# Kernel tuning notes

Hardware: AMD Instinct MI355X
Metric: run time of the kernel (lower is better)

The kernel has to match this reference:

```python
import jax, jax.numpy as jnp
import numpy as np

N_Q = 4
DEPTH = 6
DIM = 16  # 2**N_Q

# ---- fixed `design` dict (forward arg in the torch module; fixed here so the
# gate sequence is static, exercising every gate branch) ----
_K1 = ['x', 'y', 'z']
_K2 = ['H', 'Px', 'Py', 'Pz', 'CNot', 'CZ', 'Tof', 'CSwap']
DESIGN = {}
for _l in range(DEPTH):
    for _n in range(N_Q):
        DESIGN[str(_l) + str(_n) + '0'] = ((_l + _n) % 2 == 0)
        DESIGN[str(_l) + str(_n) + '1'] = _K1[(_l + _n) % 3]
        DESIGN[str(_l) + str(_n) + '2'] = _K2[(_l * N_Q + _n) % 8]

# ---- elementary gate matrices (numpy, build-time) ----
_H = np.array([[1, 1], [1, -1]], np.complex64) / np.sqrt(2.0)
_X = np.array([[0, 1], [1, 0]], np.complex64)
_Y = np.array([[0, -1j], [1j, 0]], np.complex64)
_Z = np.array([[1, 0], [0, -1]], np.complex64)
_CNOT = np.eye(4, dtype=np.complex64)[[0, 1, 3, 2]]
_CZ = np.diag(np.array([1, 1, 1, -1], np.complex64))
_TOF = np.eye(8, dtype=np.complex64)[[0, 1, 2, 3, 4, 5, 7, 6]]
_CSWAP = np.eye(8, dtype=np.complex64)[[0, 1, 2, 3, 4, 6, 5, 7]]


def _embed(gate, wires):
    # Embed a 2^k x 2^k gate acting on `wires` (wire 0 = most-significant bit,
    # PennyLane convention) into a full 16x16 unitary.
    k = len(wires)
    U = np.zeros((DIM, DIM), np.complex64)
    for i in range(DIM):
        bits = [(i >> (N_Q - 1 - q)) & 1 for q in range(N_Q)]
        sub_in = 0
        for w in wires:
            sub_in = (sub_in << 1) | bits[w]
        for sub_out in range(2 ** k):
            amp = gate[sub_out, sub_in]
            if amp != 0:
                ob = list(bits)
                for j, w in enumerate(wires):
                    ob[w] = (sub_out >> (k - 1 - j)) & 1
                o = 0
                for q in range(N_Q):
                    o = (o << 1) | ob[q]
                U[o, i] += amp
    return jnp.asarray(U)


# ---- static op list: ('fix', U16) | ('rot', kind, wire, angle_source) ----
_G1 = {'H': _H, 'Px': _X, 'Py': _Y, 'Pz': _Z}
OPS = [('fix', _embed(_H, [q])) for q in range(N_Q)]  # initial Hadamards
for _l in range(DEPTH):
    for _n in range(N_Q):
        if DESIGN[str(_l) + str(_n) + '0']:
            OPS.append(('rot', 'y', _n, ('x', _n)))  # RY(input feature)
        OPS.append(('rot', DESIGN[str(_l) + str(_n) + '1'], _n, ('w', _l, _n)))
        g = DESIGN[str(_l) + str(_n) + '2']
        if g in _G1:
            OPS.append(('fix', _embed(_G1[g], [_n])))
        elif g == 'CNot':
            OPS.append(('fix', _embed(_CNOT, [_n, (_n + 1) % N_Q])))
        elif g == 'CZ':
            OPS.append(('fix', _embed(_CZ, [_n, (_n + 1) % N_Q])))
        elif g == 'Tof':
            OPS.append(('fix', _embed(_TOF, [_n, (_n + 1) % N_Q, (_n + 2) % N_Q])))
        elif g == 'CSwap':
            OPS.append(('fix', _embed(_CSWAP, [_n, (_n + 1) % N_Q, (_n + 2) % N_Q])))


def _rot_mat(kind, th):
    # th: (B,) real angles -> (B,2,2) complex64 rotation matrices
    half = 0.5 * th
    c = jnp.cos(half).astype(jnp.complex64)
    s = jnp.sin(half).astype(jnp.complex64)
    if kind == 'x':
        m = [[c, (-1j) * s], [(-1j) * s, c]]
    elif kind == 'y':
        m = [[c, -s], [s, c]]
    else:  # 'z'
        e = jnp.exp((-1j) * half.astype(jnp.complex64))
        z = jnp.zeros_like(e)
        m = [[e, z], [z, jnp.conj(e)]]
    return jnp.stack([jnp.stack(m[0], -1), jnp.stack(m[1], -1)], -2)


def _apply_1q(state, M, q):
    # state: (B,16) complex, M: (B,2,2) complex, single-qubit gate on wire q
    B = state.shape[0]
    s = state.reshape(B, 2 ** q, 2, 2 ** (N_Q - 1 - q))
    s = jnp.einsum('bij,bajc->baic', M, s)
    return s.reshape(B, DIM)


def _run(state, x, w, adjoint):
    # adjoint: reversed gate order, negated rotation angles; all fixed gates
    # here (H, Paulis, CNOT, CZ, Toffoli, CSWAP) are Hermitian => self-adjoint.
    sign = -1.0 if adjoint else 1.0
    B = state.shape[0]
    for op in (reversed(OPS) if adjoint else OPS):
        if op[0] == 'fix':
            state = jnp.einsum('ij,bj->bi', op[1], state)
        else:
            _, kind, wire, src = op
            th = x[:, src[1]] if src[0] == 'x' else jnp.broadcast_to(w[src[1], src[2]], (B,))
            state = _apply_1q(state, _rot_mat(kind, sign * th), wire)
    return state


def _forward(x1, x2, q_params):
    w = q_params.reshape(DEPTH, N_Q)
    B = x1.shape[0]
    state = jnp.zeros((B, DIM), jnp.complex64).at[:, 0].set(1.0)
    state = _run(state, x1, w, False)   # quantum_net(x1, w)
    state = _run(state, x2, w, True)    # adjoint(quantum_net)(x2, w)
    a = state[:, 0]                     # probs[0] = |<0...0|psi>|^2
    return a.real ** 2 + a.imag ** 2


def setup_inputs():
    key = jax.random.key(0)
    k1, k2, k3 = jax.random.split(key, 3)
    B = 262144
    return {
        'x1': jax.random.normal(k1, (B, N_Q), jnp.float32),
        'x2': jax.random.normal(k2, (B, N_Q), jnp.float32),
        'q_params': jax.random.normal(k3, (DEPTH * N_Q,), jnp.float32),
    }


def reference(x1, x2, q_params):
    return _forward(x1, x2, q_params)
```

## Files before the change

### kernel.cpp

```cpp
#include <hip/hip_runtime.h>
#include <math.h>


#define DEVI static __device__ __forceinline__

typedef float f2 __attribute__((ext_vector_type(2)));

DEVI f2 nI(f2 a) { f2 r; r.x = a.y; r.y = -a.x; return r; }
DEVI f2 pI(f2 a) { f2 r; r.x = -a.y; r.y = a.x; return r; }


template<int Q> DEVI void gH(f2* v) {
  constexpr int m = 1 << (3 - Q);
  const float K = 0.70710678118654752440f;
#pragma unroll
  for (int i = 0; i < 16; ++i) if (!(i & m)) {
    const int j = i | m;
    f2 a = v[i], b = v[j];
    v[i] = (a + b) * K;
    v[j] = (a - b) * K;
  }
}

template<int Q> DEVI void gX(f2* v) {
  constexpr int m = 1 << (3 - Q);
#pragma unroll
  for (int i = 0; i < 16; ++i) if (!(i & m)) {
    const int j = i | m;
    f2 t = v[i]; v[i] = v[j]; v[j] = t;
  }
}

template<int Q> DEVI void gY(f2* v) {
  constexpr int m = 1 << (3 - Q);
#pragma unroll
  for (int i = 0; i < 16; ++i) if (!(i & m)) {
    const int j = i | m;
    f2 a = v[i], b = v[j];
    v[i] = nI(b);
    v[j] = pI(a);
  }
}

template<int Q> DEVI void gZ(f2* v) {
  constexpr int m = 1 << (3 - Q);
#pragma unroll
  for (int i = 0; i < 16; ++i) if (i & m) v[i] = -v[i];
}

template<int Q> DEVI void gRY(f2* v, float c, float s) {
  constexpr int m = 1 << (3 - Q);
#pragma unroll
  for (int i = 0; i < 16; ++i) if (!(i & m)) {
    const int j = i | m;
    f2 a = v[i], b = v[j];
    v[i] = a * c - b * s;
    v[j] = a * s + b * c;
  }
}

template<int Q> DEVI void gRX(f2* v, float c, float s) {
  constexpr int m = 1 << (3 - Q);
#pragma unroll
  for (int i = 0; i < 16; ++i) if (!(i & m)) {
    const int j = i | m;
    f2 a = v[i], b = v[j];
    v[i] = a * c + nI(b) * s;
    v[j] = b * c + nI(a) * s;
  }
}

template<int Q> DEVI void gRZ(f2* v, float c, float s) {
  constexpr int m = 1 << (3 - Q);
#pragma unroll
  for (int i = 0; i < 16; ++i) {
    f2 a = v[i];
    if (i & m) v[i] = a * c - nI(a) * s;
    else       v[i] = a * c + nI(a) * s;
  }
}

template<int C, int T> DEVI void gCNOT(f2* v) {
  constexpr int mc = 1 << (3 - C), mt = 1 << (3 - T);
#pragma unroll
  for (int i = 0; i < 16; ++i) if ((i & mc) && !(i & mt)) {
    const int j = i | mt;
    f2 t = v[i]; v[i] = v[j]; v[j] = t;
  }
}

template<int A, int B2> DEVI void gCZ(f2* v) {
  constexpr int ma = 1 << (3 - A), mb = 1 << (3 - B2);
#pragma unroll
  for (int i = 0; i < 16; ++i) if ((i & ma) && (i & mb)) v[i] = -v[i];
}

template<int C1, int C2, int T> DEVI void gTOF(f2* v) {
  constexpr int m1 = 1 << (3 - C1), m2 = 1 << (3 - C2), mt = 1 << (3 - T);
#pragma unroll
  for (int i = 0; i < 16; ++i) if ((i & m1) && (i & m2) && !(i & mt)) {
    const int j = i | mt;
    f2 t = v[i]; v[i] = v[j]; v[j] = t;
  }
}

template<int C, int A, int B2> DEVI void gCSWAP(f2* v) {
  constexpr int mc = 1 << (3 - C), ma = 1 << (3 - A), mb = 1 << (3 - B2);
#pragma unroll
  for (int i = 0; i < 16; ++i) if ((i & mc) && (i & ma) && !(i & mb)) {
    const int j = (i ^ ma) | mb;
    f2 t = v[i]; v[i] = v[j]; v[j] = t;
  }
}

DEVI float rlane(float v, int l) {
  return __int_as_float(__builtin_amdgcn_readlane(__float_as_int(v), l));
}

__global__ __launch_bounds__(256)
void qsim(const float* __restrict__ x1, const float* __restrict__ x2,
          const float* __restrict__ q, float* __restrict__ out, int B)
{
  const int b = blockIdx.x * blockDim.x + threadIdx.x;
  if (b >= B) return;

  const int lane = threadIdx.x & 63;
  float qv = 0.f;
  if (lane < 24) qv = q[lane];
  float mys, myc;
  sincosf(0.5f * qv, &mys, &myc);
  float cw[24], sw[24];
#pragma unroll
  for (int k = 0; k < 24; ++k) { cw[k] = rlane(myc, k); sw[k] = rlane(mys, k); }

  const float4 xa = reinterpret_cast<const float4*>(x1)[b];
  const float4 xb = reinterpret_cast<const float4*>(x2)[b];
  float ca[4], sa[4], cb[4], sb[4];
  __sincosf(0.5f * xa.x, &sa[0], &ca[0]);
  __sincosf(0.5f * xa.y, &sa[1], &ca[1]);
  __sincosf(0.5f * xa.z, &sa[2], &ca[2]);
  __sincosf(0.5f * xa.w, &sa[3], &ca[3]);
  __sincosf(0.5f * xb.x, &sb[0], &cb[0]);
  __sincosf(0.5f * xb.y, &sb[1], &cb[1]);
  __sincosf(0.5f * xb.z, &sb[2], &cb[2]);
  __sincosf(0.5f * xb.w, &sb[3], &cb[3]);

  f2 v[16];
#pragma unroll
  for (int i = 0; i < 16; ++i) { v[i].x = 0.f; v[i].y = 0.f; }
  v[0].x = 1.f;

  gH<0>(v); gH<1>(v); gH<2>(v); gH<3>(v);
  gRY<0>(v, ca[0], sa[0]); gRX<0>(v, cw[0],  sw[0]);  gH<0>(v);
  gRY<1>(v, cw[1], sw[1]); gX<1>(v);
  gRY<2>(v, ca[2], sa[2]); gRZ<2>(v, cw[2],  sw[2]);  gY<2>(v);
  gRX<3>(v, cw[3], sw[3]); gZ<3>(v);
  gRY<0>(v, cw[4], sw[4]); gCNOT<0,1>(v);
  gRY<1>(v, ca[1], sa[1]); gRZ<1>(v, cw[5],  sw[5]);  gCZ<1,2>(v);
  gRX<2>(v, cw[6], sw[6]); gTOF<2,3,0>(v);
  gRY<3>(v, ca[3], sa[3]); gRY<3>(v, cw[7],  sw[7]);  gCSWAP<3,0,1>(v);
  gRY<0>(v, ca[0], sa[0]); gRZ<0>(v, cw[8],  sw[8]);  gH<0>(v);
  gRX<1>(v, cw[9], sw[9]); gX<1>(v);
  gRY<2>(v, ca[2], sa[2]); gRY<2>(v, cw[10], sw[10]); gY<2>(v);
  gRZ<3>(v, cw[11], sw[11]); gZ<3>(v);
  gRX<0>(v, cw[12], sw[12]); gCNOT<0,1>(v);
  gRY<1>(v, ca[1], sa[1]); gRY<1>(v, cw[13], sw[13]); gCZ<1,2>(v);
  gRZ<2>(v, cw[14], sw[14]); gTOF<2,3,0>(v);
  gRY<3>(v, ca[3], sa[3]); gRX<3>(v, cw[15], sw[15]); gCSWAP<3,0,1>(v);
  gRY<0>(v, ca[0], sa[0]); gRY<0>(v, cw[16], sw[16]); gH<0>(v);
  gRZ<1>(v, cw[17], sw[17]); gX<1>(v);
  gRY<2>(v, ca[2], sa[2]); gRX<2>(v, cw[18], sw[18]); gY<2>(v);
  gRY<3>(v, cw[19], sw[19]); gZ<3>(v);
  gRZ<0>(v, cw[20], sw[20]); gCNOT<0,1>(v);
  gRY<1>(v, ca[1], sa[1]); gRX<1>(v, cw[21], sw[21]); gCZ<1,2>(v);
  gRY<2>(v, cw[22], sw[22]); gTOF<2,3,0>(v);
  gRY<3>(v, ca[3], sa[3]); gRZ<3>(v, cw[23], sw[23]); gCSWAP<3,0,1>(v);

  gCSWAP<3,0,1>(v); gRZ<3>(v, cw[23], -sw[23]); gRY<3>(v, cb[3], -sb[3]);
  gTOF<2,3,0>(v);   gRY<2>(v, cw[22], -sw[22]);
  gCZ<1,2>(v);      gRX<1>(v, cw[21], -sw[21]); gRY<1>(v, cb[1], -sb[1]);
  gCNOT<0,1>(v);    gRZ<0>(v, cw[20], -sw[20]);
  gZ<3>(v); gRY<3>(v, cw[19], -sw[19]);
  gY<2>(v); gRX<2>(v, cw[18], -sw[18]); gRY<2>(v, cb[2], -sb[2]);
  gX<1>(v); gRZ<1>(v, cw[17], -sw[17]);
  gH<0>(v); gRY<0>(v, cw[16], -sw[16]); gRY<0>(v, cb[0], -sb[0]);
  gCSWAP<3,0,1>(v); gRX<3>(v, cw[15], -sw[15]); gRY<3>(v, cb[3], -sb[3]);
  gTOF<2,3,0>(v);   gRZ<2>(v, cw[14], -sw[14]);
  gCZ<1,2>(v);      gRY<1>(v, cw[13], -sw[13]); gRY<1>(v, cb[1], -sb[1]);
  gCNOT<0,1>(v);    gRX<0>(v, cw[12], -sw[12]);
  gZ<3>(v); gRZ<3>(v, cw[11], -sw[11]);
  gY<2>(v); gRY<2>(v, cw[10], -sw[10]); gRY<2>(v, cb[2], -sb[2]);
  gX<1>(v); gRX<1>(v, cw[9],  -sw[9]);
  gH<0>(v); gRZ<0>(v, cw[8],  -sw[8]);  gRY<0>(v, cb[0], -sb[0]);
  gCSWAP<3,0,1>(v); gRY<3>(v, cw[7], -sw[7]); gRY<3>(v, cb[3], -sb[3]);
  gTOF<2,3,0>(v);   gRX<2>(v, cw[6], -sw[6]);
  gCZ<1,2>(v);      gRZ<1>(v, cw[5], -sw[5]); gRY<1>(v, cb[1], -sb[1]);
  gCNOT<0,1>(v);    gRY<0>(v, cw[4], -sw[4]);
  gZ<3>(v); gRX<3>(v, cw[3], -sw[3]);
  gY<2>(v); gRZ<2>(v, cw[2], -sw[2]); gRY<2>(v, cb[2], -sb[2]);
  gX<1>(v); gRY<1>(v, cw[1], -sw[1]);
  gH<0>(v); gRX<0>(v, cw[0], -sw[0]); gRY<0>(v, cb[0], -sb[0]);
  gH<3>(v); gH<2>(v); gH<1>(v); gH<0>(v);

  f2 a0 = v[0];
  out[b] = a0.x * a0.x + a0.y * a0.y;
}

extern "C" void kernel_launch(void* const* d_in, const int* in_sizes, int n_in,
                              void* d_out, int out_size, void* d_ws, size_t ws_size,
                              hipStream_t stream) {
  const float* x1 = (const float*)d_in[0];
  const float* x2 = (const float*)d_in[1];
  const float* q  = (const float*)d_in[2];
  float* out = (float*)d_out;
  const int B = in_sizes[0] / 4;
  const int block = 256;
  const int grid = (B + block - 1) / block;
  qsim<<<grid, block, 0, stream>>>(x1, x2, q, out, B);
}
```

Before: 85.15 us.

## Compute overlap as inner product of two forward states with fused gates

Instead of applying the forward circuit and then its adjoint, the kernel runs the forward circuit on both inputs and takes the inner product <U(x2)|U(x1)>. The initial Hadamards are folded into a uniform starting state, and adjacent gate pairs are fused into single kernels (H·RX, Y·RZ, Z·RX and others), including merged consecutive RY angles. Parameter sincos now uses the fast intrinsic, and launch bounds request higher occupancy. In exchange, two 16-amplitude states are live at once, which raises register pressure, and accuracy may shift slightly.

```diff
diff --git a/kernel.cpp b/kernel.cpp
--- a/kernel.cpp
+++ b/kernel.cpp
@@ -6,8 +6,9 @@
 
 typedef float f2 __attribute__((ext_vector_type(2)));
 
-DEVI f2 nI(f2 a) { f2 r; r.x = a.y; r.y = -a.x; return r; }
-DEVI f2 pI(f2 a) { f2 r; r.x = -a.y; r.y = a.x; return r; }
+DEVI f2 nI(f2 a) { f2 r; r.x = a.y;  r.y = -a.x; return r; }
+DEVI f2 pI(f2 a) { f2 r; r.x = -a.y; r.y = a.x;  return r; }
+DEVI f2 cmul(f2 a, f2 g) { return a * g.x + pI(a) * g.y; }
 
 
 template<int Q> DEVI void gH(f2* v) {
@@ -42,12 +43,6 @@
   }
 }
 
-template<int Q> DEVI void gZ(f2* v) {
-  constexpr int m = 1 << (3 - Q);
-#pragma unroll
-  for (int i = 0; i < 16; ++i) if (i & m) v[i] = -v[i];
-}
-
 template<int Q> DEVI void gRY(f2* v, float c, float s) {
   constexpr int m = 1 << (3 - Q);
 #pragma unroll
@@ -75,9 +70,107 @@
 #pragma unroll
   for (int i = 0; i < 16; ++i) {
     f2 a = v[i];
-    if (i & m) v[i] = a * c - nI(a) * s;
-    else       v[i] = a * c + nI(a) * s;
-  }
+    if (i & m) v[i] = a * c + pI(a) * s;
+    else       v[i] = a * c - pI(a) * s;
+  }
+}
+
+
+template<int Q> DEVI void gHRY(f2* v, float c, float s) {
+  constexpr int m = 1 << (3 - Q);
+  const float K = 0.70710678118654752440f;
+  const float al = K * (c + s), be = K * (c - s);
+#pragma unroll
+  for (int i = 0; i < 16; ++i) if (!(i & m)) {
+    const int j = i | m;
+    f2 a = v[i], b = v[j];
+    v[i] = a * al + b * be;
+    v[j] = a * be - b * al;
+  }
+}
+
+template<int Q> DEVI void gHRX(f2* v, f2 Em, f2 Ep) {
+  constexpr int m = 1 << (3 - Q);
+#pragma unroll
+  for (int i = 0; i < 16; ++i) if (!(i & m)) {
+    const int j = i | m;
+    f2 a = v[i], b = v[j];
+    f2 t = a + b, u = a - b;
+    v[i] = cmul(t, Em);
+    v[j] = cmul(u, Ep);
+  }
+}
+
+template<int Q> DEVI void gHRZ(f2* v, f2 Em, f2 Ep) {
+  constexpr int m = 1 << (3 - Q);
+#pragma unroll
+  for (int i = 0; i < 16; ++i) if (!(i & m)) {
+    const int j = i | m;
+    f2 a = v[i], b = v[j];
+    f2 p = cmul(a, Em), q = cmul(b, Ep);
+    v[i] = p + q;
+    v[j] = p - q;
+  }
+}
+
+template<int Q> DEVI void gYRZ(f2* v, f2 G1, f2 G2) {
+  constexpr int m = 1 << (3 - Q);
+#pragma unroll
+  for (int i = 0; i < 16; ++i) if (!(i & m)) {
+    const int j = i | m;
+    f2 a = v[i], b = v[j];
+    v[i] = cmul(b, G1);
+    v[j] = cmul(a, G2);
+  }
+}
+
+template<int Q> DEVI void gYRX(f2* v, float c, float s) {
+  constexpr int m = 1 << (3 - Q);
+#pragma unroll
+  for (int i = 0; i < 16; ++i) if (!(i & m)) {
+    const int j = i | m;
+    f2 a = v[i], b = v[j];
+    v[i] = nI(b) * c - a * s;
+    v[j] = pI(a) * c + b * s;
+  }
+}
+
+template<int Q> DEVI void gZRX(f2* v, float c, float s) {
+  constexpr int m = 1 << (3 - Q);
+#pragma unroll
+  for (int i = 0; i < 16; ++i) if (!(i & m)) {
+    const int j = i | m;
+    f2 a = v[i], b = v[j];
+    v[i] = a * c + nI(b) * s;
+    v[j] = pI(a) * s - b * c;
+  }
+}
+
+template<int Q> DEVI void gZRZ(f2* v, float c, float s) {
+  constexpr int m = 1 << (3 - Q);
+#pragma unroll
+  for (int i = 0; i < 16; ++i) {
+    f2 a = v[i];
+    if (i & m) v[i] = pI(a) * (-s) - a * c;
+    else       v[i] = a * c - pI(a) * s;
+  }
+}
+
+template<int Q> DEVI void gZRY(f2* v, float c, float s) {
+  constexpr int m = 1 << (3 - Q);
+#pragma unroll
+  for (int i = 0; i < 16; ++i) if (!(i & m)) {
+    const int j = i | m;
+    f2 a = v[i], b = v[j];
+    v[i] = a * c - b * s;
+    v[j] = a * (-s) - b * c;
+  }
+}
+
+template<int A, int B2> DEVI void gCZ(f2* v) {
+  constexpr int ma = 1 << (3 - A), mb = 1 << (3 - B2);
+#pragma unroll
+  for (int i = 0; i < 16; ++i) if ((i & ma) && (i & mb)) v[i] = -v[i];
 }
 
 template<int C, int T> DEVI void gCNOT(f2* v) {
@@ -89,12 +182,6 @@
   }
 }
 
-template<int A, int B2> DEVI void gCZ(f2* v) {
-  constexpr int ma = 1 << (3 - A), mb = 1 << (3 - B2);
-#pragma unroll
-  for (int i = 0; i < 16; ++i) if ((i & ma) && (i & mb)) v[i] = -v[i];
-}
-
 template<int C1, int C2, int T> DEVI void gTOF(f2* v) {
   constexpr int m1 = 1 << (3 - C1), m2 = 1 << (3 - C2), mt = 1 << (3 - T);
 #pragma unroll
@@ -113,11 +200,51 @@
   }
 }
 
+struct Uni {
+  float cw[24], sw[24];
+  f2 Em0, Ep0;
+  f2 G1_2, G2_2;
+  f2 Em8, Ep8;
+};
+
+DEVI void fwd(f2* v, const float* cx, const float* sx, const Uni& U) {
+  const float* cw = U.cw; const float* sw = U.sw;
+  const float c73  = cx[3]*cw[7]  - sx[3]*sw[7],  s73  = sx[3]*cw[7]  + cx[3]*sw[7];
+  const float c102 = cx[2]*cw[10] - sx[2]*sw[10], s102 = sx[2]*cw[10] + cx[2]*sw[10];
+  const float c131 = cx[1]*cw[13] - sx[1]*sw[13], s131 = sx[1]*cw[13] + cx[1]*sw[13];
+  const float c160 = cx[0]*cw[16] - sx[0]*sw[16], s160 = sx[0]*cw[16] + cx[0]*sw[16];
+
+  gRY<0>(v, cx[0], sx[0]); gHRX<0>(v, U.Em0, U.Ep0);
+  gRY<1>(v, cw[1], sw[1]); gX<1>(v);
+  gRY<2>(v, cx[2], sx[2]); gYRZ<2>(v, U.G1_2, U.G2_2);
+  gZRX<3>(v, cw[3], sw[3]);
+  gRY<0>(v, cw[4], sw[4]); gCNOT<0,1>(v);
+  gRY<1>(v, cx[1], sx[1]); gRZ<1>(v, cw[5], sw[5]); gCZ<1,2>(v);
+  gRX<2>(v, cw[6], sw[6]); gTOF<2,3,0>(v);
+  gRY<3>(v, c73, s73);     gCSWAP<3,0,1>(v);
+  gRY<0>(v, cx[0], sx[0]); gHRZ<0>(v, U.Em8, U.Ep8);
+  gRX<1>(v, cw[9], sw[9]); gX<1>(v);
+  gRY<2>(v, c102, s102);   gY<2>(v);
+  gZRZ<3>(v, cw[11], sw[11]);
+  gRX<0>(v, cw[12], sw[12]); gCNOT<0,1>(v);
+  gRY<1>(v, c131, s131);     gCZ<1,2>(v);
+  gRZ<2>(v, cw[14], sw[14]); gTOF<2,3,0>(v);
+  gRY<3>(v, cx[3], sx[3]); gRX<3>(v, cw[15], sw[15]); gCSWAP<3,0,1>(v);
+  gHRY<0>(v, c160, s160);
+  gRZ<1>(v, cw[17], sw[17]); gX<1>(v);
+  gRY<2>(v, cx[2], sx[2]); gYRX<2>(v, cw[18], sw[18]);
+  gZRY<3>(v, cw[19], sw[19]);
+  gRZ<0>(v, cw[20], sw[20]); gCNOT<0,1>(v);
+  gRY<1>(v, cx[1], sx[1]); gRX<1>(v, cw[21], sw[21]); gCZ<1,2>(v);
+  gRY<2>(v, cw[22], sw[22]); gTOF<2,3,0>(v);
+  gRY<3>(v, cx[3], sx[3]); gRZ<3>(v, cw[23], sw[23]); gCSWAP<3,0,1>(v);
+}
+
 DEVI float rlane(float v, int l) {
   return __int_as_float(__builtin_amdgcn_readlane(__float_as_int(v), l));
 }
 
-__global__ __launch_bounds__(256)
+__global__ __launch_bounds__(256, 4)
 void qsim(const float* __restrict__ x1, const float* __restrict__ x2,
           const float* __restrict__ q, float* __restrict__ out, int B)
 {
@@ -128,10 +255,18 @@
   float qv = 0.f;
   if (lane < 24) qv = q[lane];
   float mys, myc;
-  sincosf(0.5f * qv, &mys, &myc);
-  float cw[24], sw[24];
-#pragma unroll
-  for (int k = 0; k < 24; ++k) { cw[k] = rlane(myc, k); sw[k] = rlane(mys, k); }
+  __sincosf(0.5f * qv, &mys, &myc);
+
+  Uni U;
+#pragma unroll
+  for (int k = 0; k < 24; ++k) { U.cw[k] = rlane(myc, k); U.sw[k] = rlane(mys, k); }
+  const float K = 0.70710678118654752440f;
+  U.Em0.x  = K * U.cw[0]; U.Em0.y  = -K * U.sw[0];
+  U.Ep0.x  = K * U.cw[0]; U.Ep0.y  =  K * U.sw[0];
+  U.G1_2.x = U.sw[2];     U.G1_2.y = -U.cw[2];
+  U.G2_2.x = U.sw[2];     U.G2_2.y =  U.cw[2];
+  U.Em8.x  = K * U.cw[8]; U.Em8.y  = -K * U.sw[8];
+  U.Ep8.x  = K * U.cw[8]; U.Ep8.y  =  K * U.sw[8];
 
   const float4 xa = reinterpret_cast<const float4*>(x1)[b];
   const float4 xb = reinterpret_cast<const float4*>(x2)[b];
@@ -145,65 +280,20 @@
   __sincosf(0.5f * xb.z, &sb[2], &cb[2]);
   __sincosf(0.5f * xb.w, &sb[3], &cb[3]);
 
-  f2 v[16];
-#pragma unroll
-  for (int i = 0; i < 16; ++i) { v[i].x = 0.f; v[i].y = 0.f; }
-  v[0].x = 1.f;
-
-  gH<0>(v); gH<1>(v); gH<2>(v); gH<3>(v);
-  gRY<0>(v, ca[0], sa[0]); gRX<0>(v, cw[0],  sw[0]);  gH<0>(v);
-  gRY<1>(v, cw[1], sw[1]); gX<1>(v);
-  gRY<2>(v, ca[2], sa[2]); gRZ<2>(v, cw[2],  sw[2]);  gY<2>(v);
-  gRX<3>(v, cw[3], sw[3]); gZ<3>(v);
-  gRY<0>(v, cw[4], sw[4]); gCNOT<0,1>(v);
-  gRY<1>(v, ca[1], sa[1]); gRZ<1>(v, cw[5],  sw[5]);  gCZ<1,2>(v);
-  gRX<2>(v, cw[6], sw[6]); gTOF<2,3,0>(v);
-  gRY<3>(v, ca[3], sa[3]); gRY<3>(v, cw[7],  sw[7]);  gCSWAP<3,0,1>(v);
-  gRY<0>(v, ca[0], sa[0]); gRZ<0>(v, cw[8],  sw[8]);  gH<0>(v);
-  gRX<1>(v, cw[9], sw[9]); gX<1>(v);
-  gRY<2>(v, ca[2], sa[2]); gRY<2>(v, cw[10], sw[10]); gY<2>(v);
-  gRZ<3>(v, cw[11], sw[11]); gZ<3>(v);
-  gRX<0>(v, cw[12], sw[12]); gCNOT<0,1>(v);
-  gRY<1>(v, ca[1], sa[1]); gRY<1>(v, cw[13], sw[13]); gCZ<1,2>(v);
-  gRZ<2>(v, cw[14], sw[14]); gTOF<2,3,0>(v);
-  gRY<3>(v, ca[3], sa[3]); gRX<3>(v, cw[15], sw[15]); gCSWAP<3,0,1>(v);
-  gRY<0>(v, ca[0], sa[0]); gRY<0>(v, cw[16], sw[16]); gH<0>(v);
-  gRZ<1>(v, cw[17], sw[17]); gX<1>(v);
-  gRY<2>(v, ca[2], sa[2]); gRX<2>(v, cw[18], sw[18]); gY<2>(v);
-  gRY<3>(v, cw[19], sw[19]); gZ<3>(v);
-  gRZ<0>(v, cw[20], sw[20]); gCNOT<0,1>(v);
-  gRY<1>(v, ca[1], sa[1]); gRX<1>(v, cw[21], sw[21]); gCZ<1,2>(v);
-  gRY<2>(v, cw[22], sw[22]); gTOF<2,3,0>(v);
-  gRY<3>(v, ca[3], sa[3]); gRZ<3>(v, cw[23], sw[23]); gCSWAP<3,0,1>(v);
-
-  gCSWAP<3,0,1>(v); gRZ<3>(v, cw[23], -sw[23]); gRY<3>(v, cb[3], -sb[3]);
-  gTOF<2,3,0>(v);   gRY<2>(v, cw[22], -sw[22]);
-  gCZ<1,2>(v);      gRX<1>(v, cw[21], -sw[21]); gRY<1>(v, cb[1], -sb[1]);
-  gCNOT<0,1>(v);    gRZ<0>(v, cw[20], -sw[20]);
-  gZ<3>(v); gRY<3>(v, cw[19], -sw[19]);
-  gY<2>(v); gRX<2>(v, cw[18], -sw[18]); gRY<2>(v, cb[2], -sb[2]);
-  gX<1>(v); gRZ<1>(v, cw[17], -sw[17]);
-  gH<0>(v); gRY<0>(v, cw[16], -sw[16]); gRY<0>(v, cb[0], -sb[0]);
-  gCSWAP<3,0,1>(v); gRX<3>(v, cw[15], -sw[15]); gRY<3>(v, cb[3], -sb[3]);
-  gTOF<2,3,0>(v);   gRZ<2>(v, cw[14], -sw[14]);
-  gCZ<1,2>(v);      gRY<1>(v, cw[13], -sw[13]); gRY<1>(v, cb[1], -sb[1]);
-  gCNOT<0,1>(v);    gRX<0>(v, cw[12], -sw[12]);
-  gZ<3>(v); gRZ<3>(v, cw[11], -sw[11]);
-  gY<2>(v); gRY<2>(v, cw[10], -sw[10]); gRY<2>(v, cb[2], -sb[2]);
-  gX<1>(v); gRX<1>(v, cw[9],  -sw[9]);
-  gH<0>(v); gRZ<0>(v, cw[8],  -sw[8]);  gRY<0>(v, cb[0], -sb[0]);
-  gCSWAP<3,0,1>(v); gRY<3>(v, cw[7], -sw[7]); gRY<3>(v, cb[3], -sb[3]);
-  gTOF<2,3,0>(v);   gRX<2>(v, cw[6], -sw[6]);
-  gCZ<1,2>(v);      gRZ<1>(v, cw[5], -sw[5]); gRY<1>(v, cb[1], -sb[1]);
-  gCNOT<0,1>(v);    gRY<0>(v, cw[4], -sw[4]);
-  gZ<3>(v); gRX<3>(v, cw[3], -sw[3]);
-  gY<2>(v); gRZ<2>(v, cw[2], -sw[2]); gRY<2>(v, cb[2], -sb[2]);
-  gX<1>(v); gRY<1>(v, cw[1], -sw[1]);
-  gH<0>(v); gRX<0>(v, cw[0], -sw[0]); gRY<0>(v, cb[0], -sb[0]);
-  gH<3>(v); gH<2>(v); gH<1>(v); gH<0>(v);
-
-  f2 a0 = v[0];
-  out[b] = a0.x * a0.x + a0.y * a0.y;
+  f2 vA[16], vB[16];
+#pragma unroll
+  for (int i = 0; i < 16; ++i) { vA[i].x = 0.25f; vA[i].y = 0.f; vB[i].x = 0.25f; vB[i].y = 0.f; }
+
+  fwd(vA, ca, sa, U);
+  fwd(vB, cb, sb, U);
+
+  float re = 0.f, im = 0.f;
+#pragma unroll
+  for (int i = 0; i < 16; ++i) {
+    re += vB[i].x * vA[i].x + vB[i].y * vA[i].y;
+    im += vB[i].x * vA[i].y - vB[i].y * vA[i].x;
+  }
+  out[b] = re * re + im * im;
 }
 
 extern "C" void kernel_launch(void* const* d_in, const int* in_sizes, int n_in,
```

Result: faster. 81.00 us (-4.9%).
